# Performance work log

Measured on AMD Instinct MI355X. Metric: run time of the kernel, lower is better.

Reference implementation:

```python
import jax, jax.numpy as jnp
import numpy as np

B, N, J, P = 64, 2048, 32, 64   # instances, ops per instance, jobs, ops per job (N = J*P)
D, H = 128, 128                 # out_size_ope, hidden_size_ope
NEG_SLOPE = 0.2


def _kaiming(key, fan_in, fan_out):
    return jax.random.normal(key, (fan_in, fan_out), jnp.float32) * np.sqrt(2.0 / fan_in)


def _mlp(x, W1, b1, W2, b2):
    # nn.Sequential(Linear, ELU, Linear)
    return jax.nn.elu(x @ W1 + b1) @ W2 + b2


def setup_inputs() -> dict:
    key = jax.random.key(0)
    ks = jax.random.split(key, 4)
    features = jax.random.normal(ks[0], (B, N, D), jnp.float32)
    job_starts = jnp.arange(J, dtype=jnp.int32) * P                      # first op of each job block
    offsets = jax.random.randint(ks[1], (B, J), 0, P)                    # current position within block
    ope_step_batch = job_starts[None, :] + offsets                       # [B, J], step_j in [start_j, end_j]
    end_ope_biases_batch = jnp.broadcast_to(job_starts + (P - 1), (B, J))
    opes_appertain_batch = jnp.broadcast_to(jnp.repeat(jnp.arange(J, dtype=jnp.int32), P)[None, :], (B, N))
    batch_idxes = jnp.arange(B, dtype=jnp.int32)
    inp = {
        'features': features,
        'discount_r': jnp.float32(0.9),
        'ope_step_batch': ope_step_batch,
        'end_ope_biases_batch': end_ope_biases_batch,
        'opes_appertain_batch': opes_appertain_batch,
        'batch_idxes': batch_idxes,
    }
    for i, nm in enumerate(['fw', 'zj', 'pr']):
        k1, k2 = jax.random.split(jax.random.fold_in(ks[2], i))
        inp[nm + '_W1'] = _kaiming(k1, D, H)
        inp[nm + '_b1'] = jnp.zeros((H,), jnp.float32)
        inp[nm + '_W2'] = _kaiming(k2, H, D)
        inp[nm + '_b2'] = jnp.zeros((D,), jnp.float32)
    return inp


def reference(features, discount_r,
              fw_W1, fw_b1, fw_W2, fw_b2,
              zj_W1, zj_b1, zj_W2, zj_b2,
              pr_W1, pr_b1, pr_W2, pr_b2,
              ope_step_batch, end_ope_biases_batch, opes_appertain_batch, batch_idxes):
    # opes_appertain_batch is accepted but unused, exactly like the torch forward.
    f32 = features.dtype
    steps = ope_step_batch[batch_idxes]        # [B, J]
    ends = end_ope_biases_batch[batch_idxes]   # [B, J]
    i = jnp.arange(N)

    # --- per-job descending update loop, vectorized ---
    # op i is updated iff step_j < i <= end_j for its job j; descending order in the
    # original means feat[i-1] is still the ORIGINAL value, so updates are independent.
    memb = (i[None, None, :] > steps[:, :, None]) & (i[None, None, :] <= ends[:, :, None])  # [B,J,N]
    updated = jnp.any(memb, axis=1)                                                         # [B,N]
    step_of = jnp.sum(jnp.where(memb, steps[:, :, None], 0), axis=1)                        # [B,N]
    rpow = discount_r ** (i[None, :] - step_of).astype(f32)                                 # r^(i - step)
    feat_prev = jnp.concatenate([jnp.zeros_like(features[:, :1]), features[:, :-1]], axis=1)
    # aggregate(MEAN): agg_f_w(feat_pre) + agg_f_w(feat_sub * r)
    cand = _mlp(features, fw_W1, fw_b1, fw_W2, fw_b2) + \
           _mlp(feat_prev * rpow[..., None], fw_W1, fw_b1, fw_W2, fw_b2)
    feat1 = jnp.where(updated[..., None], cand, features)

    # --- collect feat at each valid job's current step (step positions are never updated) ---
    collected = jax.vmap(lambda f, s: f[s])(features, steps)   # [B, J, D]
    valid = steps <= ends                                      # [B, J]
    n = jnp.sum(valid, axis=1).astype(f32)                     # [B]
    S = jnp.sum(jnp.where(valid[..., None], collected, 0.0), axis=1)  # [B, D]
    # aggregate_dif: new[j] = agg_z_j((old[j] + r * sum_{k!=j} old[k]) / n)
    mixed = (collected + discount_r * (S[:, None, :] - collected)) / n[:, None, None]
    z = _mlp(mixed, zj_W1, zj_b1, zj_W2, zj_b2)                # [B, J, D]

    # faithful replication of feat_opt[b][save_index[k]] = features_all[k]
    # (writes at op positions equal to JOB indices 0..J-1, for valid jobs)
    head = jnp.where(valid[..., None], z, feat1[:, :J, :])
    feat2 = feat1.at[:, :J, :].set(head)

    out = jax.nn.leaky_relu(_mlp(feat2, pr_W1, pr_b1, pr_W2, pr_b2), NEG_SLOPE)
    return out
```

## Files before the change

kernel.cpp:

```cpp
#include <hip/hip_runtime.h>

#define B_ 64
#define N_ 2048
#define J_ 32
#define D_ 128
#define NEG_SLOPE_ 0.2f

typedef __attribute__((ext_vector_type(4))) float f32x4;
typedef __attribute__((ext_vector_type(8))) __bf16 bf16x8;
typedef __attribute__((ext_vector_type(4))) __bf16 bf16x4;

#define ACT_NONE 0
#define ACT_ELU 1
#define ACT_LEAKY 2

template<int ACT>
__device__ __forceinline__ float apply_act(float v) {
    if constexpr (ACT == ACT_ELU)        return v > 0.f ? v : __expf(v) - 1.f;
    else if constexpr (ACT == ACT_LEAKY) return v >= 0.f ? v : NEG_SLOPE_ * v;
    else return v;
}

__device__ __forceinline__ bf16x8 frag_ld(const __bf16* src, int row, int kc) {
    return *(const bf16x8*)&src[row * D_ + ((kc ^ (row & 7)) << 3)];
}

__device__ __forceinline__ void load_wregs2(const __bf16* __restrict__ wmat,
                                            int wst, int ln, int lq, bf16x8 wr_[4][2]) {
#pragma unroll
    for (int ks = 0; ks < 4; ++ks)
#pragma unroll
        for (int mt = 0; mt < 2; ++mt)
            wr_[ks][mt] = frag_ld(wmat, wst * 32 + mt * 16 + ln, ks * 4 + lq);
}

__device__ __forceinline__ void st_row(__bf16* dst, int row, int ch,
                                       float4 f0, float4 f1, float s) {
    bf16x8 u;
    u[0] = (__bf16)(f0.x * s); u[1] = (__bf16)(f0.y * s);
    u[2] = (__bf16)(f0.z * s); u[3] = (__bf16)(f0.w * s);
    u[4] = (__bf16)(f1.x * s); u[5] = (__bf16)(f1.y * s);
    u[6] = (__bf16)(f1.z * s); u[7] = (__bf16)(f1.w * s);
    *(bf16x8*)&dst[row * D_ + ((ch ^ (row & 7)) << 3)] = u;
}

__device__ __forceinline__ void gemmS(const __bf16* xb, const bf16x8 wr_[4][2],
                                      int ln, int lq, f32x4 acc[2][4]) {
    const f32x4 z = {0.f, 0.f, 0.f, 0.f};
#pragma unroll
    for (int mt = 0; mt < 2; ++mt)
#pragma unroll
        for (int nt = 0; nt < 4; ++nt) acc[mt][nt] = z;
#pragma unroll
    for (int ks = 0; ks < 4; ++ks) {
        const int kc = ks * 4 + lq;
        bf16x8 b[4];
#pragma unroll
        for (int nt = 0; nt < 4; ++nt) b[nt] = frag_ld(xb, nt * 16 + ln, kc);
#pragma unroll
        for (int mt = 0; mt < 2; ++mt)
#pragma unroll
            for (int nt = 0; nt < 4; ++nt)
                acc[mt][nt] = __builtin_amdgcn_mfma_f32_16x16x32_bf16(wr_[ks][mt], b[nt], acc[mt][nt], 0, 0, 0);
    }
}

template<bool INIT>
__device__ __forceinline__ void gemmS32(const __bf16* xb, const bf16x8 wr_[4][2],
                                        int ln, int lq, f32x4 acc[2][2]) {
    if constexpr (INIT) {
        const f32x4 z = {0.f, 0.f, 0.f, 0.f};
        acc[0][0] = z; acc[0][1] = z; acc[1][0] = z; acc[1][1] = z;
    }
#pragma unroll
    for (int ks = 0; ks < 4; ++ks) {
        const int kc = ks * 4 + lq;
        const bf16x8 b0 = frag_ld(xb, ln, kc);
        const bf16x8 b1 = frag_ld(xb, 16 + ln, kc);
#pragma unroll
        for (int mt = 0; mt < 2; ++mt) {
            acc[mt][0] = __builtin_amdgcn_mfma_f32_16x16x32_bf16(wr_[ks][mt], b0, acc[mt][0], 0, 0, 0);
            acc[mt][1] = __builtin_amdgcn_mfma_f32_16x16x32_bf16(wr_[ks][mt], b1, acc[mt][1], 0, 0, 0);
        }
    }
}

template<int ACT>
__device__ __forceinline__ void epiS_lds(const f32x4 acc[2][4], __bf16* dst,
                                         const float* __restrict__ bias,
                                         int wst, int ln, int lq) {
#pragma unroll
    for (int mt = 0; mt < 2; ++mt) {
        const int cb = wst * 32 + mt * 16 + lq * 4;
        const f32x4 bv = *(const f32x4*)&bias[cb];
#pragma unroll
        for (int nt = 0; nt < 4; ++nt) {
            const int jr = nt * 16 + ln;
            bf16x4 o;
#pragma unroll
            for (int r = 0; r < 4; ++r)
                o[r] = (__bf16)apply_act<ACT>(acc[mt][nt][r] + bv[r]);
            *(bf16x4*)&dst[jr * D_ + (((cb >> 3) ^ (jr & 7)) << 3) + (cb & 7)] = o;
        }
    }
}

template<int ACT>
__device__ __forceinline__ void epiS32_lds(const f32x4 acc[2][2], __bf16* dst, int rowoff,
                                           const float* __restrict__ bias,
                                           int wst, int ln, int lq) {
#pragma unroll
    for (int mt = 0; mt < 2; ++mt) {
        const int cb = wst * 32 + mt * 16 + lq * 4;
        const f32x4 bv = *(const f32x4*)&bias[cb];
#pragma unroll
        for (int nt = 0; nt < 2; ++nt) {
            const int jr = rowoff + nt * 16 + ln;
            bf16x4 o;
#pragma unroll
            for (int r = 0; r < 4; ++r)
                o[r] = (__bf16)apply_act<ACT>(acc[mt][nt][r] + bv[r]);
            *(bf16x4*)&dst[jr * D_ + (((cb >> 3) ^ (jr & 7)) << 3) + (cb & 7)] = o;
        }
    }
}

__global__ __launch_bounds__(256) void k_prep(
    const float* __restrict__ w0, const float* __restrict__ w1,
    const float* __restrict__ w2, const float* __restrict__ w3,
    const float* __restrict__ w4, const float* __restrict__ w5,
    __bf16* __restrict__ wdst,
    const float* __restrict__ F, const int* __restrict__ STEP,
    const int* __restrict__ ENDB, const int* __restrict__ BIDX,
    float* __restrict__ Sbuf, int* __restrict__ nvalid) {
    const int t = threadIdx.x;
    if (blockIdx.x < 6) {
        const float* src;
        switch (blockIdx.x) {
            case 0: src = w0; break; case 1: src = w1; break; case 2: src = w2; break;
            case 3: src = w3; break; case 4: src = w4; break; default: src = w5; break;
        }
        __bf16* d = wdst + (size_t)blockIdx.x * D_ * D_;
        for (int id = t; id < D_ * 16; id += 256) {
            const int n = id >> 4, ch = id & 15;
            bf16x8 u;
#pragma unroll
            for (int j = 0; j < 8; ++j) u[j] = (__bf16)src[(ch * 8 + j) * D_ + n];
            *(bf16x8*)&d[n * D_ + ((ch ^ (n & 7)) << 3)] = u;
        }
        return;
    }
    const int b = blockIdx.x - 6;
    __shared__ int steps_s[J_];
    __shared__ int valid_s[J_];
    __shared__ int nv;
    const int bi = BIDX[b];
    if (t == 0) nv = 0;
    __syncthreads();
    if (t < J_) {
        const int s = STEP[bi * J_ + t];
        const int e = ENDB[bi * J_ + t];
        steps_s[t] = s;
        const int v = (s <= e) ? 1 : 0;
        valid_s[t] = v;
        if (v) atomicAdd(&nv, 1);
    }
    __syncthreads();
    if (t < D_) {
        float acc = 0.f;
        for (int j = 0; j < J_; ++j)
            if (valid_s[j]) acc += F[((size_t)b * N_ + steps_s[j]) * D_ + t];
        Sbuf[b * D_ + t] = acc;
    }
    if (t == 0) nvalid[b] = nv;
}

__global__ __launch_bounds__(256, 4) void k_fused(
    const float* __restrict__ F, const float* __restrict__ rp_,
    const __bf16* __restrict__ wsW,
    const float* __restrict__ fb1, const float* __restrict__ fb2,
    const float* __restrict__ zb1, const float* __restrict__ zb2,
    const float* __restrict__ pb1, const float* __restrict__ pb2,
    const int* __restrict__ STEP, const int* __restrict__ ENDB,
    const int* __restrict__ BIDX, const float* __restrict__ Sbuf,
    const int* __restrict__ nvalid, float* __restrict__ out) {
    __shared__ __bf16 xs[64 * D_];
    __shared__ __bf16 hs[64 * D_];

    const int t = threadIdx.x;
    const int lane = t & 63, wst = t >> 6;
    const int ln = lane & 15, lq = lane >> 4;
    const int bid = blockIdx.x;
    const int b = bid >> 6, ti = bid & 63;
    const int r0 = ti * 32;
    const int bi = BIDX[b];
    const int jb = ti >> 1;
    const int s_j = STEP[bi * J_ + jb];
    const int e_j = ENDB[bi * J_ + jb];
    const float r = *rp_;
    const float l2r = __log2f(r);
    const int lo = (s_j + 1 > r0) ? s_j + 1 : r0;
    const int hi = (e_j < r0 + 31) ? e_j : r0 + 31;
    const bool has_upd = lo <= hi;
    const bool head_tile = (ti == 0);

    const float* Fb = F + (size_t)b * N_ * D_;
    const int rr_ = t >> 4;
    const int ch_ = t & 15;
    const int rA = r0 + rr_, rB = rA + 16;
    const float* qA = Fb + (size_t)rA * D_ + ch_ * 8;
    const float* qB = Fb + (size_t)rB * D_ + ch_ * 8;
    const float4 xa0 = *(const float4*)qA, xa1 = *(const float4*)(qA + 4);
    const float4 xb0 = *(const float4*)qB, xb1 = *(const float4*)(qB + 4);
    float4 ya0, ya1, yb0, yb1;
    float scA = 0.f, scB = 0.f;
    if (has_upd) {
        const bool uA = (rA > s_j) && (rA <= e_j);
        const bool uB = (rB > s_j) && (rB <= e_j);
        scA = uA ? exp2f((float)(rA - s_j) * l2r) : 0.f;
        scB = uB ? exp2f((float)(rB - s_j) * l2r) : 0.f;
        const float* uqA = Fb + (size_t)(uA ? rA - 1 : rA) * D_ + ch_ * 8;
        const float* uqB = Fb + (size_t)(uB ? rB - 1 : rB) * D_ + ch_ * 8;
        ya0 = *(const float4*)uqA; ya1 = *(const float4*)(uqA + 4);
        yb0 = *(const float4*)uqB; yb1 = *(const float4*)(uqB + 4);
    }
    bf16x8 wA[4][2];
    load_wregs2(has_upd ? wsW : wsW + 2 * 16384, wst, ln, lq, wA);

    st_row(xs, rr_, ch_, xa0, xa1, 1.f);
    st_row(xs, rr_ + 16, ch_, xb0, xb1, 1.f);
    if (has_upd) {
        st_row(xs, rr_ + 32, ch_, ya0, ya1, scA);
        st_row(xs, rr_ + 48, ch_, yb0, yb1, scB);
    }
    __syncthreads();

    if (has_upd) {
        f32x4 acc[2][4];
        gemmS(xs, wA, ln, lq, acc);
        bf16x8 wB[4][2];
        load_wregs2(wsW + 16384, wst, ln, lq, wB);
        epiS_lds<ACT_ELU>(acc, hs, fb1, wst, ln, lq);
        __syncthreads();
        f32x4 a2[2][2];
        gemmS32<true>(hs, wB, ln, lq, a2);
        gemmS32<false>(hs + 32 * D_, wB, ln, lq, a2);
#pragma unroll
        for (int nt = 0; nt < 2; ++nt) {
            const int row = nt * 16 + ln;
            const int i = r0 + row;
            if (!((i > s_j) && (i <= e_j))) continue;
#pragma unroll
            for (int mt = 0; mt < 2; ++mt) {
                const int cb = wst * 32 + mt * 16 + lq * 4;
                const f32x4 bv = *(const f32x4*)&fb2[cb];
                bf16x4 o;
#pragma unroll
                for (int rr2 = 0; rr2 < 4; ++rr2)
                    o[rr2] = (__bf16)(a2[mt][nt][rr2] + 2.f * bv[rr2]);
                *(bf16x4*)&xs[row * D_ + (((cb >> 3) ^ (row & 7)) << 3) + (cb & 7)] = o;
            }
        }
    }

    if (head_tile) {
        __syncthreads();
        const float n_ = (float)nvalid[b];
        const float inv = (n_ > 0.f) ? 1.f / n_ : 0.f;
#pragma unroll
        for (int it = 0; it < 2; ++it) {
            const int id = t + it * 256;
            const int row = id >> 4, ch = id & 15;
            const int sr = STEP[bi * J_ + row];
            const float* cr = Fb + (size_t)sr * D_ + ch * 8;
            const float4 c0 = *(const float4*)cr, c1 = *(const float4*)(cr + 4);
            const float4 s0 = *(const float4*)(Sbuf + b * D_ + ch * 8);
            const float4 s1 = *(const float4*)(Sbuf + b * D_ + ch * 8 + 4);
            bf16x8 u;
            u[0] = (__bf16)((c0.x + r * (s0.x - c0.x)) * inv);
            u[1] = (__bf16)((c0.y + r * (s0.y - c0.y)) * inv);
            u[2] = (__bf16)((c0.z + r * (s0.z - c0.z)) * inv);
            u[3] = (__bf16)((c0.w + r * (s0.w - c0.w)) * inv);
            u[4] = (__bf16)((c1.x + r * (s1.x - c1.x)) * inv);
            u[5] = (__bf16)((c1.y + r * (s1.y - c1.y)) * inv);
            u[6] = (__bf16)((c1.z + r * (s1.z - c1.z)) * inv);
            u[7] = (__bf16)((c1.w + r * (s1.w - c1.w)) * inv);
            *(bf16x8*)&hs[row * D_ + ((ch ^ (row & 7)) << 3)] = u;
        }
        __syncthreads();
        {
            bf16x8 wza[4][2];
            load_wregs2(wsW + 4 * 16384, wst, ln, lq, wza);
            f32x4 az[2][2];
            gemmS32<true>(hs, wza, ln, lq, az);
            epiS32_lds<ACT_ELU>(az, hs, 32, zb1, wst, ln, lq);
        }
        __syncthreads();
        {
            bf16x8 wzb[4][2];
            load_wregs2(wsW + 5 * 16384, wst, ln, lq, wzb);
            f32x4 az[2][2];
            gemmS32<true>(hs + 32 * D_, wzb, ln, lq, az);
#pragma unroll
            for (int nt = 0; nt < 2; ++nt) {
                const int row = nt * 16 + ln;
                const int sr = STEP[bi * J_ + row];
                const int er = ENDB[bi * J_ + row];
                if (sr > er) continue;
#pragma unroll
                for (int mt = 0; mt < 2; ++mt) {
                    const int cb = wst * 32 + mt * 16 + lq * 4;
                    const f32x4 bv = *(const f32x4*)&zb2[cb];
                    bf16x4 o;
#pragma unroll
                    for (int rr2 = 0; rr2 < 4; ++rr2)
                        o[rr2] = (__bf16)(az[mt][nt][rr2] + bv[rr2]);
                    *(bf16x4*)&xs[row * D_ + (((cb >> 3) ^ (row & 7)) << 3) + (cb & 7)] = o;
                }
            }
        }
    }

    if (has_upd || head_tile)
        load_wregs2(wsW + 2 * 16384, wst, ln, lq, wA);
    __syncthreads();

    f32x4 ap[2][2];
    gemmS32<true>(xs, wA, ln, lq, ap);
    bf16x8 wB2[4][2];
    load_wregs2(wsW + 3 * 16384, wst, ln, lq, wB2);
    epiS32_lds<ACT_ELU>(ap, hs, 0, pb1, wst, ln, lq);
    __syncthreads();

    gemmS32<true>(hs, wB2, ln, lq, ap);
    float* outb = out + ((size_t)b * N_ + r0) * D_;
#pragma unroll
    for (int mt = 0; mt < 2; ++mt) {
        const int cb = wst * 32 + mt * 16 + lq * 4;
        const f32x4 bv = *(const f32x4*)&pb2[cb];
#pragma unroll
        for (int nt = 0; nt < 2; ++nt) {
            const int jr = nt * 16 + ln;
            f32x4 o;
#pragma unroll
            for (int rr2 = 0; rr2 < 4; ++rr2)
                o[rr2] = apply_act<ACT_LEAKY>(ap[mt][nt][rr2] + bv[rr2]);
            *(f32x4*)&outb[(size_t)jr * D_ + cb] = o;
        }
    }
}

extern "C" void kernel_launch(void* const* d_in, const int* in_sizes, int n_in,
                              void* d_out, int out_size, void* d_ws, size_t ws_size,
                              hipStream_t stream) {
    const float* F    = (const float*)d_in[0];
    const float* rp   = (const float*)d_in[1];
    const int*  STEP  = (const int*)d_in[2];
    const int*  ENDB  = (const int*)d_in[3];
    const int*  BIDX  = (const int*)d_in[5];
    const float* fwW1 = (const float*)d_in[6];
    const float* fwb1 = (const float*)d_in[7];
    const float* fwW2 = (const float*)d_in[8];
    const float* fwb2 = (const float*)d_in[9];
    const float* zjW1 = (const float*)d_in[10];
    const float* zjb1 = (const float*)d_in[11];
    const float* zjW2 = (const float*)d_in[12];
    const float* zjb2 = (const float*)d_in[13];
    const float* prW1 = (const float*)d_in[14];
    const float* prb1 = (const float*)d_in[15];
    const float* prW2 = (const float*)d_in[16];
    const float* prb2 = (const float*)d_in[17];
    float* out = (float*)d_out;

    char* ws = (char*)d_ws;
    __bf16* wsW = (__bf16*)ws;
    float* Sbuf = (float*)(ws + 393216);
    int* nvalid = (int*)(ws + 425984);

    hipLaunchKernelGGL(k_prep, dim3(70), dim3(256), 0, stream,
                       fwW1, fwW2, prW1, prW2, zjW1, zjW2, wsW,
                       F, STEP, ENDB, BIDX, Sbuf, nvalid);
    hipLaunchKernelGGL(k_fused, dim3(B_ * 64), dim3(256), 0, stream,
                       F, rp, wsW, fwb1, fwb2, zjb1, zjb2, prb1, prb2,
                       STEP, ENDB, BIDX, Sbuf, nvalid, out);
}
```

Before: 64.69 us.

## Process two 32-row halves per block to reuse weight registers

Each block now covers a whole 64-row job block, two 32-row halves, so the grid shrinks from 4096 to 2048 blocks. Both halves are staged into separate LDS buffers up front, and the fw and pr weight fragments are loaded into registers once and reused for both halves. This cuts repeated weight loads and per-block setup. In exchange, LDS per block grows from 32KB to 48KB, which may lower occupancy, and the two halves run serially with extra barriers, so there are fewer blocks to hide latency.

```diff
diff --git a/kernel.cpp b/kernel.cpp
--- a/kernel.cpp
+++ b/kernel.cpp
@@ -44,6 +44,30 @@
     *(bf16x8*)&dst[row * D_ + ((ch ^ (row & 7)) << 3)] = u;
 }
 
+__device__ __forceinline__ void stage_half(__bf16* buf, const float* Fb, int row0,
+                                           bool upd, int s_j, int e_j, float l2r,
+                                           int rr_, int ch_) {
+    const int rA = row0 + rr_, rB = rA + 16;
+    const float* qA = Fb + (size_t)rA * D_ + ch_ * 8;
+    const float* qB = Fb + (size_t)rB * D_ + ch_ * 8;
+    const float4 xa0 = *(const float4*)qA, xa1 = *(const float4*)(qA + 4);
+    const float4 xb0 = *(const float4*)qB, xb1 = *(const float4*)(qB + 4);
+    st_row(buf, rr_, ch_, xa0, xa1, 1.f);
+    st_row(buf, rr_ + 16, ch_, xb0, xb1, 1.f);
+    if (upd) {
+        const bool uA = (rA > s_j) && (rA <= e_j);
+        const bool uB = (rB > s_j) && (rB <= e_j);
+        const float scA = uA ? exp2f((float)(rA - s_j) * l2r) : 0.f;
+        const float scB = uB ? exp2f((float)(rB - s_j) * l2r) : 0.f;
+        const float* uqA = Fb + (size_t)(uA ? rA - 1 : rA) * D_ + ch_ * 8;
+        const float* uqB = Fb + (size_t)(uB ? rB - 1 : rB) * D_ + ch_ * 8;
+        const float4 ya0 = *(const float4*)uqA, ya1 = *(const float4*)(uqA + 4);
+        const float4 yb0 = *(const float4*)uqB, yb1 = *(const float4*)(uqB + 4);
+        st_row(buf, rr_ + 32, ch_, ya0, ya1, scA);
+        st_row(buf, rr_ + 48, ch_, yb0, yb1, scB);
+    }
+}
+
 __device__ __forceinline__ void gemmS(const __bf16* xb, const bf16x8 wr_[4][2],
                                       int ln, int lq, f32x4 acc[2][4]) {
     const f32x4 z = {0.f, 0.f, 0.f, 0.f};
@@ -121,6 +145,27 @@
             for (int r = 0; r < 4; ++r)
                 o[r] = (__bf16)apply_act<ACT>(acc[mt][nt][r] + bv[r]);
             *(bf16x4*)&dst[jr * D_ + (((cb >> 3) ^ (jr & 7)) << 3) + (cb & 7)] = o;
+        }
+    }
+}
+
+__device__ __forceinline__ void pred_cand(const f32x4 a2[2][2], __bf16* buf, int r0h,
+                                          int s_j, int e_j, const float* __restrict__ bias,
+                                          float bscale, int wst, int ln, int lq) {
+#pragma unroll
+    for (int nt = 0; nt < 2; ++nt) {
+        const int row = nt * 16 + ln;
+        const int i = r0h + row;
+        if (!((i > s_j) && (i <= e_j))) continue;
+#pragma unroll
+        for (int mt = 0; mt < 2; ++mt) {
+            const int cb = wst * 32 + mt * 16 + lq * 4;
+            const f32x4 bv = *(const f32x4*)&bias[cb];
+            bf16x4 o;
+#pragma unroll
+            for (int rr2 = 0; rr2 < 4; ++rr2)
+                o[rr2] = (__bf16)(a2[mt][nt][rr2] + bscale * bv[rr2]);
+            *(bf16x4*)&buf[row * D_ + (((cb >> 3) ^ (row & 7)) << 3) + (cb & 7)] = o;
         }
     }
 }
@@ -184,83 +229,62 @@
     const int* __restrict__ STEP, const int* __restrict__ ENDB,
     const int* __restrict__ BIDX, const float* __restrict__ Sbuf,
     const int* __restrict__ nvalid, float* __restrict__ out) {
-    __shared__ __bf16 xs[64 * D_];
+    __shared__ __bf16 xsA[64 * D_];
+    __shared__ __bf16 xsB[64 * D_];
     __shared__ __bf16 hs[64 * D_];
 
     const int t = threadIdx.x;
     const int lane = t & 63, wst = t >> 6;
     const int ln = lane & 15, lq = lane >> 4;
     const int bid = blockIdx.x;
-    const int b = bid >> 6, ti = bid & 63;
-    const int r0 = ti * 32;
+    const int b = bid >> 5, tp = bid & 31;
+    const int r0 = tp * 64;
     const int bi = BIDX[b];
-    const int jb = ti >> 1;
-    const int s_j = STEP[bi * J_ + jb];
-    const int e_j = ENDB[bi * J_ + jb];
+    const int s_j = STEP[bi * J_ + tp];
+    const int e_j = ENDB[bi * J_ + tp];
     const float r = *rp_;
     const float l2r = __log2f(r);
-    const int lo = (s_j + 1 > r0) ? s_j + 1 : r0;
-    const int hi = (e_j < r0 + 31) ? e_j : r0 + 31;
-    const bool has_upd = lo <= hi;
-    const bool head_tile = (ti == 0);
+    const int loA = (s_j + 1 > r0) ? s_j + 1 : r0;
+    const int hiA = (e_j < r0 + 31) ? e_j : r0 + 31;
+    const bool updA = loA <= hiA;
+    const int loB = (s_j + 1 > r0 + 32) ? s_j + 1 : r0 + 32;
+    const int hiB = (e_j < r0 + 63) ? e_j : r0 + 63;
+    const bool updB = loB <= hiB;
+    const bool anyupd = updA || updB;
+    const bool head_tile = (tp == 0);
 
     const float* Fb = F + (size_t)b * N_ * D_;
-    const int rr_ = t >> 4;
-    const int ch_ = t & 15;
-    const int rA = r0 + rr_, rB = rA + 16;
-    const float* qA = Fb + (size_t)rA * D_ + ch_ * 8;
-    const float* qB = Fb + (size_t)rB * D_ + ch_ * 8;
-    const float4 xa0 = *(const float4*)qA, xa1 = *(const float4*)(qA + 4);
-    const float4 xb0 = *(const float4*)qB, xb1 = *(const float4*)(qB + 4);
-    float4 ya0, ya1, yb0, yb1;
-    float scA = 0.f, scB = 0.f;
-    if (has_upd) {
-        const bool uA = (rA > s_j) && (rA <= e_j);
-        const bool uB = (rB > s_j) && (rB <= e_j);
-        scA = uA ? exp2f((float)(rA - s_j) * l2r) : 0.f;
-        scB = uB ? exp2f((float)(rB - s_j) * l2r) : 0.f;
-        const float* uqA = Fb + (size_t)(uA ? rA - 1 : rA) * D_ + ch_ * 8;
-        const float* uqB = Fb + (size_t)(uB ? rB - 1 : rB) * D_ + ch_ * 8;
-        ya0 = *(const float4*)uqA; ya1 = *(const float4*)(uqA + 4);
-        yb0 = *(const float4*)uqB; yb1 = *(const float4*)(uqB + 4);
-    }
-    bf16x8 wA[4][2];
-    load_wregs2(has_upd ? wsW : wsW + 2 * 16384, wst, ln, lq, wA);
-
-    st_row(xs, rr_, ch_, xa0, xa1, 1.f);
-    st_row(xs, rr_ + 16, ch_, xb0, xb1, 1.f);
-    if (has_upd) {
-        st_row(xs, rr_ + 32, ch_, ya0, ya1, scA);
-        st_row(xs, rr_ + 48, ch_, yb0, yb1, scB);
-    }
-    __syncthreads();
-
-    if (has_upd) {
+    const int rr_ = t >> 4, ch_ = t & 15;
+    stage_half(xsA, Fb, r0, updA, s_j, e_j, l2r, rr_, ch_);
+    stage_half(xsB, Fb, r0 + 32, updB, s_j, e_j, l2r, rr_, ch_);
+
+    bf16x8 wf1[4][2], wf2[4][2];
+    if (anyupd) {
+        load_wregs2(wsW, wst, ln, lq, wf1);
+        load_wregs2(wsW + 16384, wst, ln, lq, wf2);
+    }
+    __syncthreads();
+
+    if (updA) {
         f32x4 acc[2][4];
-        gemmS(xs, wA, ln, lq, acc);
-        bf16x8 wB[4][2];
-        load_wregs2(wsW + 16384, wst, ln, lq, wB);
+        gemmS(xsA, wf1, ln, lq, acc);
         epiS_lds<ACT_ELU>(acc, hs, fb1, wst, ln, lq);
         __syncthreads();
         f32x4 a2[2][2];
-        gemmS32<true>(hs, wB, ln, lq, a2);
-        gemmS32<false>(hs + 32 * D_, wB, ln, lq, a2);
-#pragma unroll
-        for (int nt = 0; nt < 2; ++nt) {
-            const int row = nt * 16 + ln;
-            const int i = r0 + row;
-            if (!((i > s_j) && (i <= e_j))) continue;
-#pragma unroll
-            for (int mt = 0; mt < 2; ++mt) {
-                const int cb = wst * 32 + mt * 16 + lq * 4;
-                const f32x4 bv = *(const f32x4*)&fb2[cb];
-                bf16x4 o;
-#pragma unroll
-                for (int rr2 = 0; rr2 < 4; ++rr2)
-                    o[rr2] = (__bf16)(a2[mt][nt][rr2] + 2.f * bv[rr2]);
-                *(bf16x4*)&xs[row * D_ + (((cb >> 3) ^ (row & 7)) << 3) + (cb & 7)] = o;
-            }
-        }
+        gemmS32<true>(hs, wf2, ln, lq, a2);
+        gemmS32<false>(hs + 32 * D_, wf2, ln, lq, a2);
+        pred_cand(a2, xsA, r0, s_j, e_j, fb2, 2.f, wst, ln, lq);
+    }
+    if (updB) {
+        __syncthreads();
+        f32x4 acc[2][4];
+        gemmS(xsB, wf1, ln, lq, acc);
+        epiS_lds<ACT_ELU>(acc, hs, fb1, wst, ln, lq);
+        __syncthreads();
+        f32x4 a2[2][2];
+        gemmS32<true>(hs, wf2, ln, lq, a2);
+        gemmS32<false>(hs + 32 * D_, wf2, ln, lq, a2);
+        pred_cand(a2, xsB, r0 + 32, s_j, e_j, fb2, 2.f, wst, ln, lq);
     }
 
     if (head_tile) {
@@ -315,37 +339,61 @@
 #pragma unroll
                     for (int rr2 = 0; rr2 < 4; ++rr2)
                         o[rr2] = (__bf16)(az[mt][nt][rr2] + bv[rr2]);
-                    *(bf16x4*)&xs[row * D_ + (((cb >> 3) ^ (row & 7)) << 3) + (cb & 7)] = o;
+                    *(bf16x4*)&xsA[row * D_ + (((cb >> 3) ^ (row & 7)) << 3) + (cb & 7)] = o;
                 }
             }
         }
     }
 
-    if (has_upd || head_tile)
-        load_wregs2(wsW + 2 * 16384, wst, ln, lq, wA);
+    bf16x8 wp1[4][2];
+    load_wregs2(wsW + 2 * 16384, wst, ln, lq, wp1);
     __syncthreads();
 
     f32x4 ap[2][2];
-    gemmS32<true>(xs, wA, ln, lq, ap);
-    bf16x8 wB2[4][2];
-    load_wregs2(wsW + 3 * 16384, wst, ln, lq, wB2);
+    gemmS32<true>(xsA, wp1, ln, lq, ap);
+    bf16x8 wp2[4][2];
+    load_wregs2(wsW + 3 * 16384, wst, ln, lq, wp2);
     epiS32_lds<ACT_ELU>(ap, hs, 0, pb1, wst, ln, lq);
     __syncthreads();
-
-    gemmS32<true>(hs, wB2, ln, lq, ap);
-    float* outb = out + ((size_t)b * N_ + r0) * D_;
-#pragma unroll
-    for (int mt = 0; mt < 2; ++mt) {
-        const int cb = wst * 32 + mt * 16 + lq * 4;
-        const f32x4 bv = *(const f32x4*)&pb2[cb];
-#pragma unroll
-        for (int nt = 0; nt < 2; ++nt) {
-            const int jr = nt * 16 + ln;
-            f32x4 o;
-#pragma unroll
-            for (int rr2 = 0; rr2 < 4; ++rr2)
-                o[rr2] = apply_act<ACT_LEAKY>(ap[mt][nt][rr2] + bv[rr2]);
-            *(f32x4*)&outb[(size_t)jr * D_ + cb] = o;
+    gemmS32<true>(hs, wp2, ln, lq, ap);
+    {
+        float* outb = out + ((size_t)b * N_ + r0) * D_;
+#pragma unroll
+        for (int mt = 0; mt < 2; ++mt) {
+            const int cb = wst * 32 + mt * 16 + lq * 4;
+            const f32x4 bv = *(const f32x4*)&pb2[cb];
+#pragma unroll
+            for (int nt = 0; nt < 2; ++nt) {
+                const int jr = nt * 16 + ln;
+                f32x4 o;
+#pragma unroll
+                for (int rr2 = 0; rr2 < 4; ++rr2)
+                    o[rr2] = apply_act<ACT_LEAKY>(ap[mt][nt][rr2] + bv[rr2]);
+                *(f32x4*)&outb[(size_t)jr * D_ + cb] = o;
+            }
+        }
+    }
+    f32x4 apB[2][2];
+    gemmS32<true>(xsB, wp1, ln, lq, apB);
+    __syncthreads();
+    epiS32_lds<ACT_ELU>(apB, hs, 0, pb1, wst, ln, lq);
+    __syncthreads();
+    gemmS32<true>(hs, wp2, ln, lq, apB);
+    {
+        float* outb = out + ((size_t)b * N_ + r0 + 32) * D_;
+#pragma unroll
+        for (int mt = 0; mt < 2; ++mt) {
+            const int cb = wst * 32 + mt * 16 + lq * 4;
+            const f32x4 bv = *(const f32x4*)&pb2[cb];
+#pragma unroll
+            for (int nt = 0; nt < 2; ++nt) {
+                const int jr = nt * 16 + ln;
+                f32x4 o;
+#pragma unroll
+                for (int rr2 = 0; rr2 < 4; ++rr2)
+                    o[rr2] = apply_act<ACT_LEAKY>(apB[mt][nt][rr2] + bv[rr2]);
+                *(f32x4*)&outb[(size_t)jr * D_ + cb] = o;
+            }
         }
     }
 }
@@ -380,7 +428,7 @@
     hipLaunchKernelGGL(k_prep, dim3(70), dim3(256), 0, stream,
                        fwW1, fwW2, prW1, prW2, zjW1, zjW2, wsW,
                        F, STEP, ENDB, BIDX, Sbuf, nvalid);
-    hipLaunchKernelGGL(k_fused, dim3(B_ * 64), dim3(256), 0, stream,
+    hipLaunchKernelGGL(k_fused, dim3(B_ * 32), dim3(256), 0, stream,
                        F, rp, wsW, fwb1, fwb2, zjb1, zjb2, prb1, prb2,
                        STEP, ENDB, BIDX, Sbuf, nvalid, out);
 }
```

Result: slower. 74.02 us (+14.4%).

## Make fused kernel persistent over 8 tiles with register-resident MLP weights

Applied to the files above, without the earlier changes.

The grid shrinks from one block per 32-row tile to 512 blocks that each loop over 8 consecutive tiles. The fw and pr weight fragments are loaded into registers once and reused across those tiles, instead of being reloaded from global memory for every tile. Launch bounds drop to 2 waves per SIMD to make room for the extra weight registers. The trade-off is less parallelism and occupancy (512 blocks on a 256-CU device), and global loads are no longer overlapped with compute across independent blocks.

```diff
diff --git a/kernel.cpp b/kernel.cpp
--- a/kernel.cpp
+++ b/kernel.cpp
@@ -44,6 +44,30 @@
     *(bf16x8*)&dst[row * D_ + ((ch ^ (row & 7)) << 3)] = u;
 }
 
+__device__ __forceinline__ void stage_tile(__bf16* buf, const float* Fb, int row0,
+                                           bool upd, int s_j, int e_j, float l2r,
+                                           int rr_, int ch_) {
+    const int rA = row0 + rr_, rB = rA + 16;
+    const float* qA = Fb + (size_t)rA * D_ + ch_ * 8;
+    const float* qB = Fb + (size_t)rB * D_ + ch_ * 8;
+    const float4 xa0 = *(const float4*)qA, xa1 = *(const float4*)(qA + 4);
+    const float4 xb0 = *(const float4*)qB, xb1 = *(const float4*)(qB + 4);
+    st_row(buf, rr_, ch_, xa0, xa1, 1.f);
+    st_row(buf, rr_ + 16, ch_, xb0, xb1, 1.f);
+    if (upd) {
+        const bool uA = (rA > s_j) && (rA <= e_j);
+        const bool uB = (rB > s_j) && (rB <= e_j);
+        const float scA = uA ? exp2f((float)(rA - s_j) * l2r) : 0.f;
+        const float scB = uB ? exp2f((float)(rB - s_j) * l2r) : 0.f;
+        const float* uqA = Fb + (size_t)(uA ? rA - 1 : rA) * D_ + ch_ * 8;
+        const float* uqB = Fb + (size_t)(uB ? rB - 1 : rB) * D_ + ch_ * 8;
+        const float4 ya0 = *(const float4*)uqA, ya1 = *(const float4*)(uqA + 4);
+        const float4 yb0 = *(const float4*)uqB, yb1 = *(const float4*)(uqB + 4);
+        st_row(buf, rr_ + 32, ch_, ya0, ya1, scA);
+        st_row(buf, rr_ + 48, ch_, yb0, yb1, scB);
+    }
+}
+
 __device__ __forceinline__ void gemmS(const __bf16* xb, const bf16x8 wr_[4][2],
                                       int ln, int lq, f32x4 acc[2][4]) {
     const f32x4 z = {0.f, 0.f, 0.f, 0.f};
@@ -121,6 +145,27 @@
             for (int r = 0; r < 4; ++r)
                 o[r] = (__bf16)apply_act<ACT>(acc[mt][nt][r] + bv[r]);
             *(bf16x4*)&dst[jr * D_ + (((cb >> 3) ^ (jr & 7)) << 3) + (cb & 7)] = o;
+        }
+    }
+}
+
+__device__ __forceinline__ void pred_cand(const f32x4 a2[2][2], __bf16* buf, int r0h,
+                                          int s_j, int e_j, const float* __restrict__ bias,
+                                          float bscale, int wst, int ln, int lq) {
+#pragma unroll
+    for (int nt = 0; nt < 2; ++nt) {
+        const int row = nt * 16 + ln;
+        const int i = r0h + row;
+        if (!((i > s_j) && (i <= e_j))) continue;
+#pragma unroll
+        for (int mt = 0; mt < 2; ++mt) {
+            const int cb = wst * 32 + mt * 16 + lq * 4;
+            const f32x4 bv = *(const f32x4*)&bias[cb];
+            bf16x4 o;
+#pragma unroll
+            for (int rr2 = 0; rr2 < 4; ++rr2)
+                o[rr2] = (__bf16)(a2[mt][nt][rr2] + bscale * bv[rr2]);
+            *(bf16x4*)&buf[row * D_ + (((cb >> 3) ^ (row & 7)) << 3) + (cb & 7)] = o;
         }
     }
 }
@@ -175,7 +220,7 @@
     if (t == 0) nvalid[b] = nv;
 }
 
-__global__ __launch_bounds__(256, 4) void k_fused(
+__global__ __launch_bounds__(256, 2) void k_fused(
     const float* __restrict__ F, const float* __restrict__ rp_,
     const __bf16* __restrict__ wsW,
     const float* __restrict__ fb1, const float* __restrict__ fb2,
@@ -190,162 +235,124 @@
     const int t = threadIdx.x;
     const int lane = t & 63, wst = t >> 6;
     const int ln = lane & 15, lq = lane >> 4;
-    const int bid = blockIdx.x;
-    const int b = bid >> 6, ti = bid & 63;
-    const int r0 = ti * 32;
+    const int g = blockIdx.x;
+    const int b = g >> 3, c8 = g & 7;
     const int bi = BIDX[b];
-    const int jb = ti >> 1;
-    const int s_j = STEP[bi * J_ + jb];
-    const int e_j = ENDB[bi * J_ + jb];
     const float r = *rp_;
     const float l2r = __log2f(r);
-    const int lo = (s_j + 1 > r0) ? s_j + 1 : r0;
-    const int hi = (e_j < r0 + 31) ? e_j : r0 + 31;
-    const bool has_upd = lo <= hi;
-    const bool head_tile = (ti == 0);
-
     const float* Fb = F + (size_t)b * N_ * D_;
-    const int rr_ = t >> 4;
-    const int ch_ = t & 15;
-    const int rA = r0 + rr_, rB = rA + 16;
-    const float* qA = Fb + (size_t)rA * D_ + ch_ * 8;
-    const float* qB = Fb + (size_t)rB * D_ + ch_ * 8;
-    const float4 xa0 = *(const float4*)qA, xa1 = *(const float4*)(qA + 4);
-    const float4 xb0 = *(const float4*)qB, xb1 = *(const float4*)(qB + 4);
-    float4 ya0, ya1, yb0, yb1;
-    float scA = 0.f, scB = 0.f;
-    if (has_upd) {
-        const bool uA = (rA > s_j) && (rA <= e_j);
-        const bool uB = (rB > s_j) && (rB <= e_j);
-        scA = uA ? exp2f((float)(rA - s_j) * l2r) : 0.f;
-        scB = uB ? exp2f((float)(rB - s_j) * l2r) : 0.f;
-        const float* uqA = Fb + (size_t)(uA ? rA - 1 : rA) * D_ + ch_ * 8;
-        const float* uqB = Fb + (size_t)(uB ? rB - 1 : rB) * D_ + ch_ * 8;
-        ya0 = *(const float4*)uqA; ya1 = *(const float4*)(uqA + 4);
-        yb0 = *(const float4*)uqB; yb1 = *(const float4*)(uqB + 4);
-    }
-    bf16x8 wA[4][2];
-    load_wregs2(has_upd ? wsW : wsW + 2 * 16384, wst, ln, lq, wA);
-
-    st_row(xs, rr_, ch_, xa0, xa1, 1.f);
-    st_row(xs, rr_ + 16, ch_, xb0, xb1, 1.f);
-    if (has_upd) {
-        st_row(xs, rr_ + 32, ch_, ya0, ya1, scA);
-        st_row(xs, rr_ + 48, ch_, yb0, yb1, scB);
-    }
-    __syncthreads();
-
-    if (has_upd) {
-        f32x4 acc[2][4];
-        gemmS(xs, wA, ln, lq, acc);
-        bf16x8 wB[4][2];
-        load_wregs2(wsW + 16384, wst, ln, lq, wB);
-        epiS_lds<ACT_ELU>(acc, hs, fb1, wst, ln, lq);
+    const int rr_ = t >> 4, ch_ = t & 15;
+
+    bf16x8 wf1[4][2], wf2[4][2], wp1[4][2], wp2[4][2];
+    load_wregs2(wsW,             wst, ln, lq, wf1);
+    load_wregs2(wsW + 16384,     wst, ln, lq, wf2);
+    load_wregs2(wsW + 2 * 16384, wst, ln, lq, wp1);
+    load_wregs2(wsW + 3 * 16384, wst, ln, lq, wp2);
+
+    for (int k = 0; k < 8; ++k) {
+        const int ti = c8 * 8 + k;
+        const int r0 = ti * 32;
+        const int jb = ti >> 1;
+        const int s_j = STEP[bi * J_ + jb];
+        const int e_j = ENDB[bi * J_ + jb];
+        const int lo = (s_j + 1 > r0) ? s_j + 1 : r0;
+        const int hi = (e_j < r0 + 31) ? e_j : r0 + 31;
+        const bool upd = lo <= hi;
+        const bool head_tile = (ti == 0);
+
+        if (k) __syncthreads();
+        stage_tile(xs, Fb, r0, upd, s_j, e_j, l2r, rr_, ch_);
         __syncthreads();
-        f32x4 a2[2][2];
-        gemmS32<true>(hs, wB, ln, lq, a2);
-        gemmS32<false>(hs + 32 * D_, wB, ln, lq, a2);
-#pragma unroll
-        for (int nt = 0; nt < 2; ++nt) {
-            const int row = nt * 16 + ln;
-            const int i = r0 + row;
-            if (!((i > s_j) && (i <= e_j))) continue;
-#pragma unroll
-            for (int mt = 0; mt < 2; ++mt) {
-                const int cb = wst * 32 + mt * 16 + lq * 4;
-                const f32x4 bv = *(const f32x4*)&fb2[cb];
-                bf16x4 o;
-#pragma unroll
-                for (int rr2 = 0; rr2 < 4; ++rr2)
-                    o[rr2] = (__bf16)(a2[mt][nt][rr2] + 2.f * bv[rr2]);
-                *(bf16x4*)&xs[row * D_ + (((cb >> 3) ^ (row & 7)) << 3) + (cb & 7)] = o;
+
+        if (upd) {
+            f32x4 acc[2][4];
+            gemmS(xs, wf1, ln, lq, acc);
+            epiS_lds<ACT_ELU>(acc, hs, fb1, wst, ln, lq);
+            __syncthreads();
+            f32x4 a2[2][2];
+            gemmS32<true>(hs, wf2, ln, lq, a2);
+            gemmS32<false>(hs + 32 * D_, wf2, ln, lq, a2);
+            pred_cand(a2, xs, r0, s_j, e_j, fb2, 2.f, wst, ln, lq);
+        }
+
+        if (head_tile) {
+            __syncthreads();
+            const float n_ = (float)nvalid[b];
+            const float inv = (n_ > 0.f) ? 1.f / n_ : 0.f;
+#pragma unroll
+            for (int it = 0; it < 2; ++it) {
+                const int id = t + it * 256;
+                const int row = id >> 4, ch = id & 15;
+                const int sr = STEP[bi * J_ + row];
+                const float* cr = Fb + (size_t)sr * D_ + ch * 8;
+                const float4 c0 = *(const float4*)cr, c1 = *(const float4*)(cr + 4);
+                const float4 s0 = *(const float4*)(Sbuf + b * D_ + ch * 8);
+                const float4 s1 = *(const float4*)(Sbuf + b * D_ + ch * 8 + 4);
+                bf16x8 u;
+                u[0] = (__bf16)((c0.x + r * (s0.x - c0.x)) * inv);
+                u[1] = (__bf16)((c0.y + r * (s0.y - c0.y)) * inv);
+                u[2] = (__bf16)((c0.z + r * (s0.z - c0.z)) * inv);
+                u[3] = (__bf16)((c0.w + r * (s0.w - c0.w)) * inv);
+                u[4] = (__bf16)((c1.x + r * (s1.x - c1.x)) * inv);
+                u[5] = (__bf16)((c1.y + r * (s1.y - c1.y)) * inv);
+                u[6] = (__bf16)((c1.z + r * (s1.z - c1.z)) * inv);
+                u[7] = (__bf16)((c1.w + r * (s1.w - c1.w)) * inv);
+                *(bf16x8*)&hs[row * D_ + ((ch ^ (row & 7)) << 3)] = u;
             }
-        }
-    }
-
-    if (head_tile) {
-        __syncthreads();
-        const float n_ = (float)nvalid[b];
-        const float inv = (n_ > 0.f) ? 1.f / n_ : 0.f;
-#pragma unroll
-        for (int it = 0; it < 2; ++it) {
-            const int id = t + it * 256;
-            const int row = id >> 4, ch = id & 15;
-            const int sr = STEP[bi * J_ + row];
-            const float* cr = Fb + (size_t)sr * D_ + ch * 8;
-            const float4 c0 = *(const float4*)cr, c1 = *(const float4*)(cr + 4);
-            const float4 s0 = *(const float4*)(Sbuf + b * D_ + ch * 8);
-            const float4 s1 = *(const float4*)(Sbuf + b * D_ + ch * 8 + 4);
-            bf16x8 u;
-            u[0] = (__bf16)((c0.x + r * (s0.x - c0.x)) * inv);
-            u[1] = (__bf16)((c0.y + r * (s0.y - c0.y)) * inv);
-            u[2] = (__bf16)((c0.z + r * (s0.z - c0.z)) * inv);
-            u[3] = (__bf16)((c0.w + r * (s0.w - c0.w)) * inv);
-            u[4] = (__bf16)((c1.x + r * (s1.x - c1.x)) * inv);
-            u[5] = (__bf16)((c1.y + r * (s1.y - c1.y)) * inv);
-            u[6] = (__bf16)((c1.z + r * (s1.z - c1.z)) * inv);
-            u[7] = (__bf16)((c1.w + r * (s1.w - c1.w)) * inv);
-            *(bf16x8*)&hs[row * D_ + ((ch ^ (row & 7)) << 3)] = u;
-        }
-        __syncthreads();
-        {
-            bf16x8 wza[4][2];
-            load_wregs2(wsW + 4 * 16384, wst, ln, lq, wza);
-            f32x4 az[2][2];
-            gemmS32<true>(hs, wza, ln, lq, az);
-            epiS32_lds<ACT_ELU>(az, hs, 32, zb1, wst, ln, lq);
-        }
-        __syncthreads();
-        {
-            bf16x8 wzb[4][2];
-            load_wregs2(wsW + 5 * 16384, wst, ln, lq, wzb);
-            f32x4 az[2][2];
-            gemmS32<true>(hs + 32 * D_, wzb, ln, lq, az);
-#pragma unroll
-            for (int nt = 0; nt < 2; ++nt) {
-                const int row = nt * 16 + ln;
-                const int sr = STEP[bi * J_ + row];
-                const int er = ENDB[bi * J_ + row];
-                if (sr > er) continue;
-#pragma unroll
-                for (int mt = 0; mt < 2; ++mt) {
-                    const int cb = wst * 32 + mt * 16 + lq * 4;
-                    const f32x4 bv = *(const f32x4*)&zb2[cb];
-                    bf16x4 o;
-#pragma unroll
-                    for (int rr2 = 0; rr2 < 4; ++rr2)
-                        o[rr2] = (__bf16)(az[mt][nt][rr2] + bv[rr2]);
-                    *(bf16x4*)&xs[row * D_ + (((cb >> 3) ^ (row & 7)) << 3) + (cb & 7)] = o;
+            __syncthreads();
+            load_wregs2(wsW + 4 * 16384, wst, ln, lq, wp1);
+            {
+                f32x4 az[2][2];
+                gemmS32<true>(hs, wp1, ln, lq, az);
+                epiS32_lds<ACT_ELU>(az, hs, 32, zb1, wst, ln, lq);
+            }
+            __syncthreads();
+            load_wregs2(wsW + 5 * 16384, wst, ln, lq, wp2);
+            {
+                f32x4 az[2][2];
+                gemmS32<true>(hs + 32 * D_, wp2, ln, lq, az);
+#pragma unroll
+                for (int nt = 0; nt < 2; ++nt) {
+                    const int row = nt * 16 + ln;
+                    const int sr = STEP[bi * J_ + row];
+                    const int er = ENDB[bi * J_ + row];
+                    if (sr > er) continue;
+#pragma unroll
+                    for (int mt = 0; mt < 2; ++mt) {
+                        const int cb = wst * 32 + mt * 16 + lq * 4;
+                        const f32x4 bv = *(const f32x4*)&zb2[cb];
+                        bf16x4 o;
+#pragma unroll
+                        for (int rr2 = 0; rr2 < 4; ++rr2)
+                            o[rr2] = (__bf16)(az[mt][nt][rr2] + bv[rr2]);
+                        *(bf16x4*)&xs[row * D_ + (((cb >> 3) ^ (row & 7)) << 3) + (cb & 7)] = o;
+                    }
                 }
             }
-        }
-    }
-
-    if (has_upd || head_tile)
-        load_wregs2(wsW + 2 * 16384, wst, ln, lq, wA);
-    __syncthreads();
-
-    f32x4 ap[2][2];
-    gemmS32<true>(xs, wA, ln, lq, ap);
-    bf16x8 wB2[4][2];
-    load_wregs2(wsW + 3 * 16384, wst, ln, lq, wB2);
-    epiS32_lds<ACT_ELU>(ap, hs, 0, pb1, wst, ln, lq);
-    __syncthreads();
-
-    gemmS32<true>(hs, wB2, ln, lq, ap);
-    float* outb = out + ((size_t)b * N_ + r0) * D_;
-#pragma unroll
-    for (int mt = 0; mt < 2; ++mt) {
-        const int cb = wst * 32 + mt * 16 + lq * 4;
-        const f32x4 bv = *(const f32x4*)&pb2[cb];
-#pragma unroll
-        for (int nt = 0; nt < 2; ++nt) {
-            const int jr = nt * 16 + ln;
-            f32x4 o;
-#pragma unroll
-            for (int rr2 = 0; rr2 < 4; ++rr2)
-                o[rr2] = apply_act<ACT_LEAKY>(ap[mt][nt][rr2] + bv[rr2]);
-            *(f32x4*)&outb[(size_t)jr * D_ + cb] = o;
+            load_wregs2(wsW + 2 * 16384, wst, ln, lq, wp1);
+            load_wregs2(wsW + 3 * 16384, wst, ln, lq, wp2);
+        }
+        __syncthreads();
+
+        f32x4 ap[2][2];
+        gemmS32<true>(xs, wp1, ln, lq, ap);
+        epiS32_lds<ACT_ELU>(ap, hs, 0, pb1, wst, ln, lq);
+        __syncthreads();
+        gemmS32<true>(hs, wp2, ln, lq, ap);
+        float* outb = out + ((size_t)b * N_ + r0) * D_;
+#pragma unroll
+        for (int mt = 0; mt < 2; ++mt) {
+            const int cb = wst * 32 + mt * 16 + lq * 4;
+            const f32x4 bv = *(const f32x4*)&pb2[cb];
+#pragma unroll
+            for (int nt = 0; nt < 2; ++nt) {
+                const int jr = nt * 16 + ln;
+                f32x4 o;
+#pragma unroll
+                for (int rr2 = 0; rr2 < 4; ++rr2)
+                    o[rr2] = apply_act<ACT_LEAKY>(ap[mt][nt][rr2] + bv[rr2]);
+                *(f32x4*)&outb[(size_t)jr * D_ + cb] = o;
+            }
         }
     }
 }
@@ -380,7 +387,7 @@
     hipLaunchKernelGGL(k_prep, dim3(70), dim3(256), 0, stream,
                        fwW1, fwW2, prW1, prW2, zjW1, zjW2, wsW,
                        F, STEP, ENDB, BIDX, Sbuf, nvalid);
-    hipLaunchKernelGGL(k_fused, dim3(B_ * 64), dim3(256), 0, stream,
+    hipLaunchKernelGGL(k_fused, dim3(512), dim3(256), 0, stream,
                        F, rp, wsW, fwb1, fwb2, zjb1, zjb2, prb1, prb2,
                        STEP, ENDB, BIDX, Sbuf, nvalid, out);
 }
```

After: 81.13 us. 25.4% more time.
